# Kernel tuning notes

Hardware: AMD Instinct MI355X
Metric: run time of the kernel (lower is better)

The kernel has to match this reference:

```python
import math
import jax, jax.numpy as jnp
import numpy as np

B, L, T, D, H, SD = 8, 512, 512, 768, 12, 5


def setup_inputs() -> dict:
    key = jax.random.key(0)
    ks = jax.random.split(key, 16)
    s = 0.02
    return {
        "q": jax.random.normal(ks[0], (B, L, D), jnp.float32),
        "k": jax.random.normal(ks[1], (B, T, D), jnp.float32),
        "v": jax.random.normal(ks[2], (B, T, D), jnp.float32),
        "pairwise_locs": jax.random.normal(ks[3], (B, L, T, SD), jnp.float32),
        "key_padding_mask": jax.random.randint(ks[4], (B, T), 0, 2).astype(bool),
        "Wq": jax.random.normal(ks[5], (D, D), jnp.float32) * s,
        "bq": jnp.zeros((D,), jnp.float32),
        "Wk": jax.random.normal(ks[6], (D, D), jnp.float32) * s,
        "bk": jnp.zeros((D,), jnp.float32),
        "Wv": jax.random.normal(ks[7], (D, D), jnp.float32) * s,
        "bv": jnp.zeros((D,), jnp.float32),
        "Wl": jax.random.normal(ks[8], (D, H * (SD + 1)), jnp.float32) * s,
        "bl": jnp.zeros((H * (SD + 1),), jnp.float32),
        "Wf": jax.random.normal(ks[9], (D, D), jnp.float32) * s,
        "bf": jnp.zeros((D,), jnp.float32),
    }


def reference(q, k, v, pairwise_locs, key_padding_mask,
              Wq, bq, Wk, bk, Wv, bv, Wl, bl, Wf, bf):
    b, l, d = q.shape
    t = k.shape[1]
    sd = pairwise_locs.shape[-1]
    h = Wl.shape[1] // (sd + 1)          # spatial_multihead=True -> h == n_head
    dh = d // h

    # projections -> [h, b, seq, dh]
    qh = (q @ Wq + bq).reshape(b, l, h, dh).transpose(2, 0, 1, 3)
    kh = (k @ Wk + bk).reshape(b, t, h, dh).transpose(2, 0, 1, 3)
    vh = (v @ Wv + bv).reshape(b, t, h, dh).transpose(2, 0, 1, 3)

    attn = jnp.einsum('hblk,hbtk->hblt', qh, kh) / math.sqrt(dh)

    # language-conditioned spatial weights from residual (= q input)
    sw = (q @ Wl + bl).reshape(b, l, h, sd + 1).transpose(2, 0, 1, 3)  # [h,b,l,sd+1]
    spatial_bias = sw[..., :1]
    spatial_w = sw[..., 1:]
    loc_attn = jax.nn.sigmoid(
        jnp.einsum('hbld,bltd->hblt', spatial_w, pairwise_locs) + spatial_bias)

    mask = key_padding_mask[None, :, None, :]          # [1,b,1,t]
    attn = jnp.where(mask, -jnp.inf, attn)
    loc_attn = jnp.where(mask, 0.0, loc_attn)

    fused_attn = jax.nn.softmax(jnp.log(jnp.clip(loc_attn, 1e-6)) + attn, axis=3)

    out = jnp.einsum('hblt,hbtv->hblv', fused_attn, vh)
    out = out.transpose(1, 2, 0, 3).reshape(b, l, d)
    out = out @ Wf + bf
    return (out, fused_attn)
```

## Files before the change

### kernel.cpp

```cpp
#include <hip/hip_runtime.h>
#include <hip/hip_bf16.h>

#define B_ 8
#define L_ 512
#define T_ 512
#define D_ 768
#define H_ 12
#define DH_ 64
#define SD_ 5
#define NSW_ 72
#define K2_ 1536
#define K3_ 2304

typedef __attribute__((ext_vector_type(8))) short bf16x8;
typedef __attribute__((ext_vector_type(4))) float f32x4;
typedef unsigned short ushort_t;

__device__ __forceinline__ unsigned short f2bf(float x) {
    union { __hip_bfloat16 h; unsigned short u; } cv;
    cv.h = __float2bfloat16(x);
    return cv.u;
}
__device__ __forceinline__ float bf2f(unsigned short u) {
    union { unsigned short u; __hip_bfloat16 h; } cv;
    cv.u = u;
    return __bfloat162float(cv.h);
}

__device__ __forceinline__ void gload_lds16(const void* g, void* l) {
    __builtin_amdgcn_global_load_lds((const __attribute__((address_space(1))) void*)g,
                                     (__attribute__((address_space(3))) void*)l,
                                     16, 0, 0);
}

__global__ __launch_bounds__(256) void asplit_kernel(
    const float* __restrict__ q, const float* __restrict__ k, const float* __restrict__ v,
    short* __restrict__ q2, short* __restrict__ k2, short* __restrict__ v2)
{
    const int z = blockIdx.z;
    const float* A = (z == 0) ? q : (z == 1) ? k : v;
    short* O = (z == 0) ? q2 : (z == 1) ? k2 : v2;
    const int col = blockIdx.x * 256 + threadIdx.x;
    const int m   = blockIdx.y;
    if (col >= D_) return;
    const float a = A[(size_t)m * D_ + col];
    const unsigned short hi = f2bf(a);
    const unsigned short lo = f2bf(a - bf2f(hi));
    O[(size_t)m * K2_ + col]       = (short)hi;
    O[(size_t)m * K2_ + D_ + col]  = (short)lo;
}

__global__ __launch_bounds__(256) void wsplit_kernel(
    const float* __restrict__ Wq, const float* __restrict__ Wk,
    const float* __restrict__ Wv, const float* __restrict__ Wl,
    const float* __restrict__ Wf,
    short* __restrict__ WqT3, short* __restrict__ WkT3, short* __restrict__ WvT3,
    short* __restrict__ WlT3, short* __restrict__ WfT3)
{
    const int z = blockIdx.z;
    const float* W; short* O; int Nw, Npad;
    if (z == 0)      { W = Wq; O = WqT3; Nw = D_;   Npad = 768; }
    else if (z == 1) { W = Wk; O = WkT3; Nw = D_;   Npad = 768; }
    else if (z == 2) { W = Wv; O = WvT3; Nw = D_;   Npad = 768; }
    else if (z == 3) { W = Wl; O = WlT3; Nw = NSW_; Npad = 128; }
    else             { W = Wf; O = WfT3; Nw = D_;   Npad = 768; }

    const int k0 = blockIdx.x * 64;
    const int n0 = blockIdx.y * 64;
    if (n0 >= Npad) return;

    __shared__ float sm[64][65];
    const int c  = threadIdx.x & 63;
    const int r4 = threadIdx.x >> 6;

#pragma unroll
    for (int i = 0; i < 16; i++) {
        const int r = i * 4 + r4;
        float val = 0.f;
        if (n0 + c < Nw) val = W[(size_t)(k0 + r) * Nw + n0 + c];
        sm[r][c] = val;
    }
    __syncthreads();

#pragma unroll
    for (int i = 0; i < 16; i++) {
        const int nl = i * 4 + r4;
        const int n  = n0 + nl;
        if (n >= Npad) continue;
        const float v = (n < Nw) ? sm[c][nl] : 0.f;
        const unsigned short hi = f2bf(v);
        const unsigned short lo = f2bf(v - bf2f(hi));
        const size_t rb = (size_t)n * K3_;
        O[rb + k0 + c]        = (short)hi;
        O[rb + 768 + k0 + c]  = (short)lo;
        O[rb + 1536 + k0 + c] = (short)hi;
    }
}

__global__ __launch_bounds__(256) void mfma_gemm(
    const short* __restrict__ q2, const short* __restrict__ k2, const short* __restrict__ v2,
    const short* __restrict__ WqT3, const short* __restrict__ WkT3,
    const short* __restrict__ WvT3, const short* __restrict__ WlT3,
    const short* __restrict__ WfT3,
    const float* __restrict__ bq, const float* __restrict__ bk,
    const float* __restrict__ bv, const float* __restrict__ bl,
    const float* __restrict__ bf,
    const short* __restrict__ outp2,
    ushort_t* __restrict__ qs2a, ushort_t* __restrict__ ks2a, ushort_t* __restrict__ vt2,
    float* __restrict__ swv, float* __restrict__ outf,
    int zoff)
{
    const int z = zoff + blockIdx.z;
    const short* A2; const short* WT3; const float* bias;
    if (z == 0)      { A2 = q2;    WT3 = WqT3; bias = bq; }
    else if (z == 1) { A2 = k2;    WT3 = WkT3; bias = bk; }
    else if (z == 2) { A2 = v2;    WT3 = WvT3; bias = bv; }
    else if (z == 3) { A2 = q2;    WT3 = WlT3; bias = bl; }
    else             { A2 = outp2; WT3 = WfT3; bias = bf; }

    if (z == 3 && blockIdx.x != 0) return;

    const int m0 = blockIdx.y * 128;
    const int n0 = blockIdx.x * 128;

    __shared__ __align__(16) short As[128 * 32];
    __shared__ __align__(16) short Bs[128 * 32];

    const int tid  = threadIdx.x;
    const int lane = tid & 63;
    const int wv_  = tid >> 6;
    const int wm   = (wv_ & 1) << 6;
    const int wn   = (wv_ >> 1) << 6;
    const int l15  = lane & 15;
    const int quad = lane >> 4;

    f32x4 acc[4][4] = {};

    const int sa  = tid;
    const int sb  = tid + 256;
    const int ra  = sa >> 2, ka = (sa & 3) << 3;
    const int rb  = sb >> 2, kb8 = (sb & 3) << 3;

    for (int kb = 0; kb < K3_; kb += 32) {
        const int akb = (kb < 768) ? kb : kb - 768;
        __syncthreads();
        gload_lds16(A2  + (size_t)(m0 + ra) * K2_ + akb + ka,  &As[sa << 3]);
        gload_lds16(A2  + (size_t)(m0 + rb) * K2_ + akb + kb8, &As[sb << 3]);
        gload_lds16(WT3 + (size_t)(n0 + ra) * K3_ + kb  + ka,  &Bs[sa << 3]);
        gload_lds16(WT3 + (size_t)(n0 + rb) * K3_ + kb  + kb8, &Bs[sb << 3]);
        __syncthreads();

        bf16x8 af[4], bfr[4];
#pragma unroll
        for (int t = 0; t < 4; t++) {
            af[t]  = *(const bf16x8*)&As[(wm + t * 16 + l15) * 32 + quad * 8];
            bfr[t] = *(const bf16x8*)&Bs[(wn + t * 16 + l15) * 32 + quad * 8];
        }
#pragma unroll
        for (int mt = 0; mt < 4; mt++)
#pragma unroll
            for (int nt = 0; nt < 4; nt++)
                acc[mt][nt] = __builtin_amdgcn_mfma_f32_16x16x32_bf16(
                    af[mt], bfr[nt], acc[mt][nt], 0, 0, 0);
    }

    if (z <= 2) {
        ushort_t* dst = (z == 0) ? qs2a : (z == 1) ? ks2a : vt2;
#pragma unroll
        for (int nt = 0; nt < 4; nt++) {
            const int col = n0 + wn + nt * 16 + l15;
            const int hh = col >> 6, dd = col & 63;
            const float bvv = bias[col];
#pragma unroll
            for (int mt = 0; mt < 4; mt++) {
                const int rowb = m0 + wm + mt * 16 + quad * 4;
                if (z < 2) {
#pragma unroll
                    for (int r = 0; r < 4; r++) {
                        const int gr = rowb + r;
                        const int bb = gr >> 9, ll = gr & 511;
                        const float x = acc[mt][nt][r] + bvv;
                        const ushort_t hi = f2bf(x);
                        const ushort_t lo = f2bf(x - bf2f(hi));
                        const size_t base = (((size_t)hh * B_ + bb) * 512 + ll) * 128 + dd;
                        dst[base]      = hi;
                        dst[base + 64] = lo;
                    }
                } else {
                    const int bb = rowb >> 9, tt = rowb & 511;
                    ushort_t hi4[4], lo4[4];
#pragma unroll
                    for (int r = 0; r < 4; r++) {
                        const float x = acc[mt][nt][r] + bvv;
                        hi4[r] = f2bf(x);
                        lo4[r] = f2bf(x - bf2f(hi4[r]));
                    }
                    const size_t base = (((size_t)hh * B_ + bb) * 128 + dd) * 512 + tt;
                    *(ushort4*)&dst[base]            = *(ushort4*)hi4;
                    *(ushort4*)&dst[base + 64 * 512] = *(ushort4*)lo4;
                }
            }
        }
    } else if (z == 3) {
#pragma unroll
        for (int nt = 0; nt < 4; nt++) {
            const int col = n0 + wn + nt * 16 + l15;
            if (col >= NSW_) continue;
            const float bvv = bias[col];
#pragma unroll
            for (int mt = 0; mt < 4; mt++) {
                const int row = m0 + wm + mt * 16 + quad * 4;
#pragma unroll
                for (int r = 0; r < 4; r++)
                    swv[(size_t)(row + r) * NSW_ + col] = acc[mt][nt][r] + bvv;
            }
        }
    } else {
#pragma unroll
        for (int nt = 0; nt < 4; nt++) {
            const int col = n0 + wn + nt * 16 + l15;
            const float bvv = bias[col];
#pragma unroll
            for (int mt = 0; mt < 4; mt++) {
                const int row = m0 + wm + mt * 16 + quad * 4;
#pragma unroll
                for (int r = 0; r < 4; r++)
                    outf[(size_t)(row + r) * D_ + col] = acc[mt][nt][r] + bvv;
            }
        }
    }
}

__global__ __launch_bounds__(256) void sig_kernel(
    const float* __restrict__ ploc, const float* __restrict__ swv,
    const int* __restrict__ maskp, _Float16* __restrict__ sig16)
{
    const int b = blockIdx.y;
    const int l = blockIdx.x;
    const int tid = threadIdx.x;

    __shared__ float pls[512 * 5];
    __shared__ float sws[72];
    __shared__ int   msk[512];

    const float* src = ploc + (size_t)(b * 512 + l) * 512 * 5;
    for (int i = tid; i < 640; i += 256)
        *(float4*)&pls[i * 4] = *(const float4*)(src + i * 4);
    if (tid < 72) sws[tid] = swv[(size_t)(b * 512 + l) * NSW_ + tid];
    for (int i = tid; i < 512; i += 256) msk[i] = maskp[b * 512 + i];
    __syncthreads();

    for (int e = tid; e < H_ * 512; e += 256) {
        const int t  = e & 511;
        const int hh = e >> 9;
        float s = sws[hh * 6];
#pragma unroll
        for (int d = 0; d < SD_; d++) s += sws[hh * 6 + 1 + d] * pls[t * 5 + d];
        const float sig = msk[t] ? 0.f : fmaxf(1.f / (1.f + __expf(-s)), 1e-6f);
        sig16[(((size_t)hh * B_ + b) * 512 + l) * 512 + t] = (_Float16)sig;
    }
}

__global__ __launch_bounds__(256) void attn_kernel(
    const ushort_t* __restrict__ qs2, const ushort_t* __restrict__ ks2,
    const ushort_t* __restrict__ vt2, const _Float16* __restrict__ sig16,
    float* __restrict__ fused, ushort_t* __restrict__ outp2,
    float* __restrict__ sums)
{
    const int h  = blockIdx.z;
    const int b  = blockIdx.y;
    const int l0 = blockIdx.x << 6;
    const int hb = h * B_ + b;
    const int tid  = threadIdx.x;
    const int lane = tid & 63;
    const int wv   = tid >> 6;
    const int l15  = lane & 15;
    const int quad = lane >> 4;

    __shared__ __align__(16) ushort_t qs[64 * 128];
    __shared__ __align__(16) ushort_t ks[64 * 128];
    __shared__ __align__(16) ushort_t vts[128 * 64];
    __shared__ __align__(16) ushort_t ps[64 * 136];
    __shared__ float ssb[4 * 64];
    __shared__ float ssum[64];

    {
        const size_t qbase = ((size_t)hb * 512 + l0) * 128;
#pragma unroll
        for (int j = 0; j < 4; j++) {
            const int i = tid + 256 * j;
            const int r = i >> 4, c = i & 15, gc = c ^ (r & 7);
            gload_lds16(qs2 + qbase + r * 128 + gc * 8, &qs[i * 8]);
        }
    }

    float pacc = 0.f;
    f32x4 accpv[4] = {};

    for (int t0 = 0; t0 < T_; t0 += 64) {
        __syncthreads();
        {
            const size_t kbase = ((size_t)hb * 512 + t0) * 128;
#pragma unroll
            for (int j = 0; j < 4; j++) {
                const int i = tid + 256 * j;
                const int r = i >> 4, c = i & 15, gc = c ^ (r & 7);
                gload_lds16(ks2 + kbase + r * 128 + gc * 8, &ks[i * 8]);
            }
            const size_t vbase = (size_t)hb * 128 * 512;
#pragma unroll
            for (int j = 0; j < 4; j++) {
                const int i = tid + 256 * j;
                const int r = i >> 3, c = i & 7, gc = c ^ (r & 7);
                gload_lds16(vt2 + vbase + (size_t)r * 512 + t0 + gc * 8, &vts[i * 8]);
            }
        }
        __syncthreads();

        float sigv[4][4];
        {
            const _Float16* sgp = sig16 + (((size_t)hb * 512 + l0) * 512) + t0 + wv * 16 + l15;
#pragma unroll
            for (int mt = 0; mt < 4; mt++)
#pragma unroll
                for (int r2 = 0; r2 < 4; r2++)
                    sigv[mt][r2] = (float)sgp[(size_t)(mt * 16 + quad * 4 + r2) * 512];
        }

        f32x4 acq[4] = {};
        {
            const int trow = wv * 16 + l15;
            const int tsw  = trow & 7;
            const bf16x8 bk0 = *(const bf16x8*)&ks[trow * 128 + ((0  + quad) ^ tsw) * 8];
            const bf16x8 bk1 = *(const bf16x8*)&ks[trow * 128 + ((4  + quad) ^ tsw) * 8];
            const bf16x8 bk2 = *(const bf16x8*)&ks[trow * 128 + ((8  + quad) ^ tsw) * 8];
            const bf16x8 bk3 = *(const bf16x8*)&ks[trow * 128 + ((12 + quad) ^ tsw) * 8];
#pragma unroll
            for (int mt = 0; mt < 4; mt++) {
                const int arow = mt * 16 + l15;
                const int asw  = arow & 7;
                const bf16x8 a0 = *(const bf16x8*)&qs[arow * 128 + ((0  + quad) ^ asw) * 8];
                const bf16x8 a1 = *(const bf16x8*)&qs[arow * 128 + ((4  + quad) ^ asw) * 8];
                const bf16x8 a2 = *(const bf16x8*)&qs[arow * 128 + ((8  + quad) ^ asw) * 8];
                const bf16x8 a3 = *(const bf16x8*)&qs[arow * 128 + ((12 + quad) ^ asw) * 8];
                f32x4 a = acq[mt];
                a = __builtin_amdgcn_mfma_f32_16x16x32_bf16(a0, bk0, a, 0, 0, 0);
                a = __builtin_amdgcn_mfma_f32_16x16x32_bf16(a1, bk1, a, 0, 0, 0);
                a = __builtin_amdgcn_mfma_f32_16x16x32_bf16(a0, bk2, a, 0, 0, 0);
                a = __builtin_amdgcn_mfma_f32_16x16x32_bf16(a1, bk3, a, 0, 0, 0);
                a = __builtin_amdgcn_mfma_f32_16x16x32_bf16(a2, bk0, a, 0, 0, 0);
                a = __builtin_amdgcn_mfma_f32_16x16x32_bf16(a3, bk1, a, 0, 0, 0);
                acq[mt] = a;
            }
        }

        {
            const int tcol = wv * 16 + l15;
#pragma unroll
            for (int mt = 0; mt < 4; mt++)
#pragma unroll
                for (int r2 = 0; r2 < 4; r2++) {
                    const int lrow = mt * 16 + quad * 4 + r2;
                    const float p  = sigv[mt][r2] * __expf(acq[mt][r2] * 0.125f);
                    const ushort_t hi = f2bf(p);
                    const ushort_t lo = f2bf(p - bf2f(hi));
                    ps[lrow * 136 + tcol]      = hi;
                    ps[lrow * 136 + 64 + tcol] = lo;
                }
        }
        __syncthreads();

        {
            const int row = tid >> 2, c4 = tid & 3;
            float vbuf[16];
            float s = 0.f;
#pragma unroll
            for (int jj = 0; jj < 16; jj++) {
                const int t = c4 * 16 + jj;
                const float pv = bf2f(ps[row * 136 + t]) + bf2f(ps[row * 136 + 64 + t]);
                vbuf[jj] = pv;
                s += pv;
            }
            pacc += s;
            float* dstf = fused + ((size_t)hb * 512 + l0 + row) * 512 + t0 + c4 * 16;
#pragma unroll
            for (int jj = 0; jj < 4; jj++)
                *(float4*)(dstf + jj * 4) = *(float4*)&vbuf[jj * 4];
        }

        {
            const int vrh = wv * 16 + l15;
            const int vrl = 64 + vrh;
            const int swh = vrh & 7, swl = vrl & 7;
            const bf16x8 bh0 = *(const bf16x8*)&vts[vrh * 64 + ((0 + quad) ^ swh) * 8];
            const bf16x8 bh1 = *(const bf16x8*)&vts[vrh * 64 + ((4 + quad) ^ swh) * 8];
            const bf16x8 bl0 = *(const bf16x8*)&vts[vrl * 64 + ((0 + quad) ^ swl) * 8];
            const bf16x8 bl1 = *(const bf16x8*)&vts[vrl * 64 + ((4 + quad) ^ swl) * 8];
#pragma unroll
            for (int mt = 0; mt < 4; mt++) {
                const int prow = mt * 16 + l15;
                const bf16x8 ph0 = *(const bf16x8*)&ps[prow * 136 + 0  + quad * 8];
                const bf16x8 ph1 = *(const bf16x8*)&ps[prow * 136 + 32 + quad * 8];
                const bf16x8 pl0 = *(const bf16x8*)&ps[prow * 136 + 64 + quad * 8];
                const bf16x8 pl1 = *(const bf16x8*)&ps[prow * 136 + 96 + quad * 8];
                f32x4 a = accpv[mt];
                a = __builtin_amdgcn_mfma_f32_16x16x32_bf16(ph0, bh0, a, 0, 0, 0);
                a = __builtin_amdgcn_mfma_f32_16x16x32_bf16(ph1, bh1, a, 0, 0, 0);
                a = __builtin_amdgcn_mfma_f32_16x16x32_bf16(ph0, bl0, a, 0, 0, 0);
                a = __builtin_amdgcn_mfma_f32_16x16x32_bf16(ph1, bl1, a, 0, 0, 0);
                a = __builtin_amdgcn_mfma_f32_16x16x32_bf16(pl0, bh0, a, 0, 0, 0);
                a = __builtin_amdgcn_mfma_f32_16x16x32_bf16(pl1, bh1, a, 0, 0, 0);
                accpv[mt] = a;
            }
        }
    }

    __syncthreads();
    ssb[(tid & 3) * 64 + (tid >> 2)] = pacc;
    __syncthreads();
    if (tid < 64) {
        const float s = ssb[tid] + ssb[64 + tid] + ssb[128 + tid] + ssb[192 + tid];
        ssum[tid] = s;
        sums[(size_t)hb * 512 + l0 + tid] = s;
    }
    __syncthreads();

#pragma unroll
    for (int mt = 0; mt < 4; mt++)
#pragma unroll
        for (int r2 = 0; r2 < 4; r2++) {
            const int lrow = mt * 16 + quad * 4 + r2;
            const float val = accpv[mt][r2] / ssum[lrow];
            const ushort_t hi = f2bf(val);
            const ushort_t lo = f2bf(val - bf2f(hi));
            const size_t obase = ((size_t)(b * 512 + l0 + lrow)) * K2_ + h * 64 + wv * 16 + l15;
            outp2[obase]       = hi;
            outp2[obase + D_]  = lo;
        }
}

__global__ __launch_bounds__(256) void norm_kernel(
    float* __restrict__ fused, const float* __restrict__ sums)
{
    const int gi = blockIdx.x * 256 + threadIdx.x;
    float4* f4 = (float4*)fused;
    float4 v = f4[gi];
    const float inv = 1.f / sums[gi >> 7];
    v.x *= inv; v.y *= inv; v.z *= inv; v.w *= inv;
    f4[gi] = v;
}

extern "C" void kernel_launch(void* const* d_in, const int* in_sizes, int n_in,
                              void* d_out, int out_size, void* d_ws, size_t ws_size,
                              hipStream_t stream) {
    const float* q    = (const float*)d_in[0];
    const float* k    = (const float*)d_in[1];
    const float* v    = (const float*)d_in[2];
    const float* ploc = (const float*)d_in[3];
    const int*   mask = (const int*)  d_in[4];
    const float* Wq   = (const float*)d_in[5];
    const float* bq   = (const float*)d_in[6];
    const float* Wk   = (const float*)d_in[7];
    const float* bk   = (const float*)d_in[8];
    const float* Wv   = (const float*)d_in[9];
    const float* bv   = (const float*)d_in[10];
    const float* Wl   = (const float*)d_in[11];
    const float* bl   = (const float*)d_in[12];
    const float* Wf   = (const float*)d_in[13];
    const float* bf   = (const float*)d_in[14];

    char* base = (char*)d_ws;
    short*    q2    = (short*)(base + 0);
    short*    k2    = (short*)(base + 12582912);
    short*    v2    = (short*)(base + 25165824);
    short*    WqT3  = (short*)(base + 37748736);
    short*    WkT3  = (short*)(base + 41287680);
    short*    WvT3  = (short*)(base + 44826624);
    short*    WlT3  = (short*)(base + 48365568);
    _Float16* sig16 = (_Float16*)(base + 0);
    short*    WfT3  = (short*)(base + 50331648);
    ushort_t* qs2a  = (ushort_t*)(base + 53870592);
    ushort_t* ks2a  = (ushort_t*)(base + 66453504);
    ushort_t* vt2   = (ushort_t*)(base + 79036416);
    float*    swv   = (float*)(base + 91619328);
    float*    sums  = (float*)(base + 92798976);
    short*    outp2 = (short*)(base + 92995584);

    float* out   = (float*)d_out;
    float* fused = out + (size_t)4096 * D_;

    asplit_kernel<<<dim3(3, 4096, 3), 256, 0, stream>>>(q, k, v, q2, k2, v2);
    wsplit_kernel<<<dim3(12, 12, 5), 256, 0, stream>>>(
        Wq, Wk, Wv, Wl, Wf, WqT3, WkT3, WvT3, WlT3, WfT3);

    mfma_gemm<<<dim3(6, 32, 4), 256, 0, stream>>>(
        q2, k2, v2, WqT3, WkT3, WvT3, WlT3, WfT3,
        bq, bk, bv, bl, bf, outp2, qs2a, ks2a, vt2, swv, out, 0);

    sig_kernel<<<dim3(512, 8), 256, 0, stream>>>(ploc, swv, mask, sig16);

    attn_kernel<<<dim3(8, 8, 12), 256, 0, stream>>>(
        qs2a, ks2a, vt2, sig16, fused, (ushort_t*)outp2, sums);

    norm_kernel<<<dim3(24576), 256, 0, stream>>>(fused, sums);

    mfma_gemm<<<dim3(6, 32, 1), 256, 0, stream>>>(
        q2, k2, v2, WqT3, WkT3, WvT3, WlT3, WfT3,
        bq, bk, bv, bl, bf, outp2, qs2a, ks2a, vt2, swv, out, 4);
}
```

Before: 511.4 us.

## Split-K projection and output GEMMs with atomics, fuse normalization into attention

```diff
diff --git a/kernel.cpp b/kernel.cpp
--- a/kernel.cpp
+++ b/kernel.cpp
@@ -31,6 +31,17 @@
     __builtin_amdgcn_global_load_lds((const __attribute__((address_space(1))) void*)g,
                                      (__attribute__((address_space(3))) void*)l,
                                      16, 0, 0);
+}
+
+__global__ __launch_bounds__(256) void zero_kernel(float4* __restrict__ p) {
+    p[(size_t)blockIdx.x * 256 + threadIdx.x] = make_float4(0.f, 0.f, 0.f, 0.f);
+}
+
+__global__ __launch_bounds__(256) void bias_init(
+    float4* __restrict__ out4, const float4* __restrict__ bf4)
+{
+    const size_t idx = (size_t)blockIdx.x * 256 + threadIdx.x;
+    out4[idx] = bf4[idx % 192];
 }
 
 __global__ __launch_bounds__(256) void asplit_kernel(
@@ -97,31 +108,24 @@
     }
 }
 
-__global__ __launch_bounds__(256) void mfma_gemm(
+__global__ __launch_bounds__(256, 4) void proj_gemm(
     const short* __restrict__ q2, const short* __restrict__ k2, const short* __restrict__ v2,
     const short* __restrict__ WqT3, const short* __restrict__ WkT3,
     const short* __restrict__ WvT3, const short* __restrict__ WlT3,
-    const short* __restrict__ WfT3,
-    const float* __restrict__ bq, const float* __restrict__ bk,
-    const float* __restrict__ bv, const float* __restrict__ bl,
-    const float* __restrict__ bf,
-    const short* __restrict__ outp2,
-    ushort_t* __restrict__ qs2a, ushort_t* __restrict__ ks2a, ushort_t* __restrict__ vt2,
-    float* __restrict__ swv, float* __restrict__ outf,
-    int zoff)
-{
-    const int z = zoff + blockIdx.z;
-    const short* A2; const short* WT3; const float* bias;
-    if (z == 0)      { A2 = q2;    WT3 = WqT3; bias = bq; }
-    else if (z == 1) { A2 = k2;    WT3 = WkT3; bias = bk; }
-    else if (z == 2) { A2 = v2;    WT3 = WvT3; bias = bv; }
-    else if (z == 3) { A2 = q2;    WT3 = WlT3; bias = bl; }
-    else             { A2 = outp2; WT3 = WfT3; bias = bf; }
-
-    if (z == 3 && blockIdx.x != 0) return;
+    float* __restrict__ Cp, float* __restrict__ Cpsw)
+{
+    const int z = blockIdx.z;
+    int g, part, bx = blockIdx.x;
+    if (z < 6) { g = z >> 1; part = z & 1; }
+    else       { if (bx >= 2) return; g = 3; part = bx; bx = 0; }
+
+    const short* A2  = (g == 1) ? k2 : (g == 2) ? v2 : q2;
+    const short* WT3 = (g == 0) ? WqT3 : (g == 1) ? WkT3 : (g == 2) ? WvT3 : WlT3;
+    float* C   = (g < 3) ? (Cp + (size_t)g * 4096 * 768) : Cpsw;
+    const int Ncols = (g < 3) ? 768 : NSW_;
 
     const int m0 = blockIdx.y * 128;
-    const int n0 = blockIdx.x * 128;
+    const int n0 = bx * 128;
 
     __shared__ __align__(16) short As[128 * 32];
     __shared__ __align__(16) short Bs[128 * 32];
@@ -141,7 +145,8 @@
     const int ra  = sa >> 2, ka = (sa & 3) << 3;
     const int rb  = sb >> 2, kb8 = (sb & 3) << 3;
 
-    for (int kb = 0; kb < K3_; kb += 32) {
+    const int kbeg = part * 1152;
+    for (int kb = kbeg; kb < kbeg + 1152; kb += 32) {
         const int akb = (kb < 768) ? kb : kb - 768;
         __syncthreads();
         gload_lds16(A2  + (size_t)(m0 + ra) * K2_ + akb + ka,  &As[sa << 3]);
@@ -164,71 +169,167 @@
                     af[mt], bfr[nt], acc[mt][nt], 0, 0, 0);
     }
 
-    if (z <= 2) {
-        ushort_t* dst = (z == 0) ? qs2a : (z == 1) ? ks2a : vt2;
-#pragma unroll
-        for (int nt = 0; nt < 4; nt++) {
-            const int col = n0 + wn + nt * 16 + l15;
-            const int hh = col >> 6, dd = col & 63;
-            const float bvv = bias[col];
-#pragma unroll
-            for (int mt = 0; mt < 4; mt++) {
-                const int rowb = m0 + wm + mt * 16 + quad * 4;
-                if (z < 2) {
-#pragma unroll
-                    for (int r = 0; r < 4; r++) {
-                        const int gr = rowb + r;
-                        const int bb = gr >> 9, ll = gr & 511;
-                        const float x = acc[mt][nt][r] + bvv;
-                        const ushort_t hi = f2bf(x);
-                        const ushort_t lo = f2bf(x - bf2f(hi));
-                        const size_t base = (((size_t)hh * B_ + bb) * 512 + ll) * 128 + dd;
-                        dst[base]      = hi;
-                        dst[base + 64] = lo;
-                    }
-                } else {
-                    const int bb = rowb >> 9, tt = rowb & 511;
-                    ushort_t hi4[4], lo4[4];
-#pragma unroll
-                    for (int r = 0; r < 4; r++) {
-                        const float x = acc[mt][nt][r] + bvv;
-                        hi4[r] = f2bf(x);
-                        lo4[r] = f2bf(x - bf2f(hi4[r]));
-                    }
-                    const size_t base = (((size_t)hh * B_ + bb) * 128 + dd) * 512 + tt;
-                    *(ushort4*)&dst[base]            = *(ushort4*)hi4;
-                    *(ushort4*)&dst[base + 64 * 512] = *(ushort4*)lo4;
-                }
-            }
-        }
-    } else if (z == 3) {
-#pragma unroll
-        for (int nt = 0; nt < 4; nt++) {
-            const int col = n0 + wn + nt * 16 + l15;
-            if (col >= NSW_) continue;
-            const float bvv = bias[col];
-#pragma unroll
-            for (int mt = 0; mt < 4; mt++) {
-                const int row = m0 + wm + mt * 16 + quad * 4;
-#pragma unroll
-                for (int r = 0; r < 4; r++)
-                    swv[(size_t)(row + r) * NSW_ + col] = acc[mt][nt][r] + bvv;
-            }
-        }
-    } else {
-#pragma unroll
-        for (int nt = 0; nt < 4; nt++) {
-            const int col = n0 + wn + nt * 16 + l15;
-            const float bvv = bias[col];
-#pragma unroll
-            for (int mt = 0; mt < 4; mt++) {
-                const int row = m0 + wm + mt * 16 + quad * 4;
-#pragma unroll
-                for (int r = 0; r < 4; r++)
-                    outf[(size_t)(row + r) * D_ + col] = acc[mt][nt][r] + bvv;
-            }
-        }
-    }
+#pragma unroll
+    for (int nt = 0; nt < 4; nt++) {
+        const int col = n0 + wn + nt * 16 + l15;
+        if (col >= Ncols) continue;
+#pragma unroll
+        for (int mt = 0; mt < 4; mt++) {
+            const int rowb = m0 + wm + mt * 16 + quad * 4;
+#pragma unroll
+            for (int r = 0; r < 4; r++)
+                unsafeAtomicAdd(&C[(size_t)(rowb + r) * Ncols + col], acc[mt][nt][r]);
+        }
+    }
+}
+
+__global__ __launch_bounds__(256, 4) void final_gemm(
+    const short* __restrict__ A2, const short* __restrict__ WT3,
+    float* __restrict__ out)
+{
+    const int part = blockIdx.z;
+    const int m0 = blockIdx.y * 128;
+    const int n0 = blockIdx.x * 128;
+
+    __shared__ __align__(16) short As[128 * 32];
+    __shared__ __align__(16) short Bs[128 * 32];
+
+    const int tid  = threadIdx.x;
+    const int lane = tid & 63;
+    const int wv_  = tid >> 6;
+    const int wm   = (wv_ & 1) << 6;
+    const int wn   = (wv_ >> 1) << 6;
+    const int l15  = lane & 15;
+    const int quad = lane >> 4;
+
+    f32x4 acc[4][4] = {};
+
+    const int sa  = tid;
+    const int sb  = tid + 256;
+    const int ra  = sa >> 2, ka = (sa & 3) << 3;
+    const int rb  = sb >> 2, kb8 = (sb & 3) << 3;
+
+    const int kbeg = part * 576;
+    for (int kb = kbeg; kb < kbeg + 576; kb += 32) {
+        const int akb = (kb < 768) ? kb : kb - 768;
+        __syncthreads();
+        gload_lds16(A2  + (size_t)(m0 + ra) * K2_ + akb + ka,  &As[sa << 3]);
+        gload_lds16(A2  + (size_t)(m0 + rb) * K2_ + akb + kb8, &As[sb << 3]);
+        gload_lds16(WT3 + (size_t)(n0 + ra) * K3_ + kb  + ka,  &Bs[sa << 3]);
+        gload_lds16(WT3 + (size_t)(n0 + rb) * K3_ + kb  + kb8, &Bs[sb << 3]);
+        __syncthreads();
+
+        bf16x8 af[4], bfr[4];
+#pragma unroll
+        for (int t = 0; t < 4; t++) {
+            af[t]  = *(const bf16x8*)&As[(wm + t * 16 + l15) * 32 + quad * 8];
+            bfr[t] = *(const bf16x8*)&Bs[(wn + t * 16 + l15) * 32 + quad * 8];
+        }
+#pragma unroll
+        for (int mt = 0; mt < 4; mt++)
+#pragma unroll
+            for (int nt = 0; nt < 4; nt++)
+                acc[mt][nt] = __builtin_amdgcn_mfma_f32_16x16x32_bf16(
+                    af[mt], bfr[nt], acc[mt][nt], 0, 0, 0);
+    }
+
+#pragma unroll
+    for (int nt = 0; nt < 4; nt++) {
+        const int col = n0 + wn + nt * 16 + l15;
+#pragma unroll
+        for (int mt = 0; mt < 4; mt++) {
+            const int rowb = m0 + wm + mt * 16 + quad * 4;
+#pragma unroll
+            for (int r = 0; r < 4; r++)
+                unsafeAtomicAdd(&out[(size_t)(rowb + r) * D_ + col], acc[mt][nt][r]);
+        }
+    }
+}
+
+__global__ __launch_bounds__(256) void convert_qk(
+    const float* __restrict__ Cp, const float* __restrict__ bq,
+    const float* __restrict__ bk,
+    ushort_t* __restrict__ qs2a, ushort_t* __restrict__ ks2a)
+{
+    const int g = blockIdx.z;
+    const float* src  = Cp + (size_t)g * 4096 * 768;
+    const float* bias = g ? bk : bq;
+    ushort_t* dst = g ? ks2a : qs2a;
+    const int r0 = blockIdx.x * 8;
+
+#pragma unroll
+    for (int j = 0; j < 6; j++) {
+        const int idx = threadIdx.x + 256 * j;
+        const int row = r0 + idx / 192;
+        const int c4  = (idx % 192) * 4;
+        float4 x = *(const float4*)&src[(size_t)row * 768 + c4];
+        const float4 b4 = *(const float4*)&bias[c4];
+        x.x += b4.x; x.y += b4.y; x.z += b4.z; x.w += b4.w;
+        const int hh = c4 >> 6, dd = c4 & 63;
+        const int bb = row >> 9, ll = row & 511;
+        const size_t base = (((size_t)hh * B_ + bb) * 512 + ll) * 128 + dd;
+        ushort_t hi[4], lo[4];
+        const float xv[4] = {x.x, x.y, x.z, x.w};
+#pragma unroll
+        for (int u = 0; u < 4; u++) {
+            hi[u] = f2bf(xv[u]);
+            lo[u] = f2bf(xv[u] - bf2f(hi[u]));
+        }
+        *(ushort4*)&dst[base]      = *(ushort4*)hi;
+        *(ushort4*)&dst[base + 64] = *(ushort4*)lo;
+    }
+}
+
+__global__ __launch_bounds__(256) void convert_v(
+    const float* __restrict__ Cp, const float* __restrict__ bv,
+    ushort_t* __restrict__ vt2)
+{
+    const int t0 = blockIdx.x * 64;
+    const int b  = blockIdx.y;
+    const int h  = blockIdx.z;
+    const float* src = Cp + (size_t)2 * 4096 * 768;
+
+    __shared__ float sm[64][65];
+    const int tid = threadIdx.x;
+    {
+        const int r = tid >> 2, cseg = (tid & 3) * 16;
+        const size_t rowb = (size_t)(b * 512 + t0 + r) * 768 + h * 64 + cseg;
+#pragma unroll
+        for (int u = 0; u < 4; u++) {
+            float4 x = *(const float4*)&src[rowb + u * 4];
+            sm[r][cseg + u * 4 + 0] = x.x;
+            sm[r][cseg + u * 4 + 1] = x.y;
+            sm[r][cseg + u * 4 + 2] = x.z;
+            sm[r][cseg + u * 4 + 3] = x.w;
+        }
+    }
+    __syncthreads();
+    {
+        const int c = tid >> 2, seg = (tid & 3) * 16;
+        const float bvv = bv[h * 64 + c];
+        ushort_t hib[16], lob[16];
+#pragma unroll
+        for (int i = 0; i < 16; i++) {
+            const float val = sm[seg + i][c] + bvv;
+            hib[i] = f2bf(val);
+            lob[i] = f2bf(val - bf2f(hib[i]));
+        }
+        const size_t bh = (((size_t)h * B_ + b) * 128 + c) * 512 + t0 + seg;
+        const size_t bl = bh + (size_t)64 * 512;
+#pragma unroll
+        for (int u = 0; u < 4; u++) {
+            *(ushort4*)&vt2[bh + u * 4] = *(ushort4*)&hib[u * 4];
+            *(ushort4*)&vt2[bl + u * 4] = *(ushort4*)&lob[u * 4];
+        }
+    }
+}
+
+__global__ __launch_bounds__(256) void convert_sw(
+    const float* __restrict__ Cpsw, const float* __restrict__ bl,
+    float* __restrict__ swv)
+{
+    const int idx = blockIdx.x * 256 + threadIdx.x;
+    swv[idx] = Cpsw[idx] + bl[idx % NSW_];
 }
 
 __global__ __launch_bounds__(256) void sig_kernel(
@@ -261,11 +362,10 @@
     }
 }
 
-__global__ __launch_bounds__(256) void attn_kernel(
+__global__ __launch_bounds__(256, 3) void attn_kernel(
     const ushort_t* __restrict__ qs2, const ushort_t* __restrict__ ks2,
     const ushort_t* __restrict__ vt2, const _Float16* __restrict__ sig16,
-    float* __restrict__ fused, ushort_t* __restrict__ outp2,
-    float* __restrict__ sums)
+    float* __restrict__ fused, ushort_t* __restrict__ outp2)
 {
     const int h  = blockIdx.z;
     const int b  = blockIdx.y;
@@ -277,20 +377,21 @@
     const int l15  = lane & 15;
     const int quad = lane >> 4;
 
-    __shared__ __align__(16) ushort_t qs[64 * 128];
     __shared__ __align__(16) ushort_t ks[64 * 128];
     __shared__ __align__(16) ushort_t vts[128 * 64];
     __shared__ __align__(16) ushort_t ps[64 * 136];
     __shared__ float ssb[4 * 64];
     __shared__ float ssum[64];
 
+    bf16x8 aq[4][4];
     {
         const size_t qbase = ((size_t)hb * 512 + l0) * 128;
 #pragma unroll
-        for (int j = 0; j < 4; j++) {
-            const int i = tid + 256 * j;
-            const int r = i >> 4, c = i & 15, gc = c ^ (r & 7);
-            gload_lds16(qs2 + qbase + r * 128 + gc * 8, &qs[i * 8]);
+        for (int mt = 0; mt < 4; mt++) {
+            const size_t rb = qbase + (size_t)(mt * 16 + l15) * 128;
+#pragma unroll
+            for (int c = 0; c < 4; c++)
+                aq[mt][c] = *(const bf16x8*)(qs2 + rb + (c * 4 + quad) * 8);
         }
     }
 
@@ -337,19 +438,13 @@
             const bf16x8 bk3 = *(const bf16x8*)&ks[trow * 128 + ((12 + quad) ^ tsw) * 8];
 #pragma unroll
             for (int mt = 0; mt < 4; mt++) {
-                const int arow = mt * 16 + l15;
-                const int asw  = arow & 7;
-                const bf16x8 a0 = *(const bf16x8*)&qs[arow * 128 + ((0  + quad) ^ asw) * 8];
-                const bf16x8 a1 = *(const bf16x8*)&qs[arow * 128 + ((4  + quad) ^ asw) * 8];
-                const bf16x8 a2 = *(const bf16x8*)&qs[arow * 128 + ((8  + quad) ^ asw) * 8];
-                const bf16x8 a3 = *(const bf16x8*)&qs[arow * 128 + ((12 + quad) ^ asw) * 8];
                 f32x4 a = acq[mt];
-                a = __builtin_amdgcn_mfma_f32_16x16x32_bf16(a0, bk0, a, 0, 0, 0);
-                a = __builtin_amdgcn_mfma_f32_16x16x32_bf16(a1, bk1, a, 0, 0, 0);
-                a = __builtin_amdgcn_mfma_f32_16x16x32_bf16(a0, bk2, a, 0, 0, 0);
-                a = __builtin_amdgcn_mfma_f32_16x16x32_bf16(a1, bk3, a, 0, 0, 0);
-                a = __builtin_amdgcn_mfma_f32_16x16x32_bf16(a2, bk0, a, 0, 0, 0);
-                a = __builtin_amdgcn_mfma_f32_16x16x32_bf16(a3, bk1, a, 0, 0, 0);
+                a = __builtin_amdgcn_mfma_f32_16x16x32_bf16(aq[mt][0], bk0, a, 0, 0, 0);
+                a = __builtin_amdgcn_mfma_f32_16x16x32_bf16(aq[mt][1], bk1, a, 0, 0, 0);
+                a = __builtin_amdgcn_mfma_f32_16x16x32_bf16(aq[mt][0], bk2, a, 0, 0, 0);
+                a = __builtin_amdgcn_mfma_f32_16x16x32_bf16(aq[mt][1], bk3, a, 0, 0, 0);
+                a = __builtin_amdgcn_mfma_f32_16x16x32_bf16(aq[mt][2], bk0, a, 0, 0, 0);
+                a = __builtin_amdgcn_mfma_f32_16x16x32_bf16(aq[mt][3], bk1, a, 0, 0, 0);
                 acq[mt] = a;
             }
         }
@@ -419,11 +514,23 @@
     ssb[(tid & 3) * 64 + (tid >> 2)] = pacc;
     __syncthreads();
     if (tid < 64) {
-        const float s = ssb[tid] + ssb[64 + tid] + ssb[128 + tid] + ssb[192 + tid];
-        ssum[tid] = s;
-        sums[(size_t)hb * 512 + l0 + tid] = s;
+        ssum[tid] = ssb[tid] + ssb[64 + tid] + ssb[128 + tid] + ssb[192 + tid];
     }
     __syncthreads();
+
+    {
+        const int row = tid >> 2, c4 = tid & 3;
+        const float inv = 1.f / ssum[row];
+        float* frow = fused + ((size_t)hb * 512 + l0 + row) * 512 + c4 * 16;
+        for (int t0 = 0; t0 < T_; t0 += 64) {
+#pragma unroll
+            for (int jj = 0; jj < 4; jj++) {
+                float4 x = *(float4*)(frow + t0 + jj * 4);
+                x.x *= inv; x.y *= inv; x.z *= inv; x.w *= inv;
+                *(float4*)(frow + t0 + jj * 4) = x;
+            }
+        }
+    }
 
 #pragma unroll
     for (int mt = 0; mt < 4; mt++)
@@ -437,17 +544,6 @@
             outp2[obase]       = hi;
             outp2[obase + D_]  = lo;
         }
-}
-
-__global__ __launch_bounds__(256) void norm_kernel(
-    float* __restrict__ fused, const float* __restrict__ sums)
-{
-    const int gi = blockIdx.x * 256 + threadIdx.x;
-    float4* f4 = (float4*)fused;
-    float4 v = f4[gi];
-    const float inv = 1.f / sums[gi >> 7];
-    v.x *= inv; v.y *= inv; v.z *= inv; v.w *= inv;
-    f4[gi] = v;
 }
 
 extern "C" void kernel_launch(void* const* d_in, const int* in_sizes, int n_in,
@@ -477,34 +573,37 @@
     short*    WkT3  = (short*)(base + 41287680);
     short*    WvT3  = (short*)(base + 44826624);
     short*    WlT3  = (short*)(base + 48365568);
-    _Float16* sig16 = (_Float16*)(base + 0);
-    short*    WfT3  = (short*)(base + 50331648);
-    ushort_t* qs2a  = (ushort_t*)(base + 53870592);
-    ushort_t* ks2a  = (ushort_t*)(base + 66453504);
-    ushort_t* vt2   = (ushort_t*)(base + 79036416);
-    float*    swv   = (float*)(base + 91619328);
-    float*    sums  = (float*)(base + 92798976);
-    short*    outp2 = (short*)(base + 92995584);
+    short*    WfT3  = (short*)(base + 48955392);
+    float*    Cp    = (float*)(base + 52494336);
+    float*    Cpsw  = (float*)(base + 90243072);
+    ushort_t* qs2a  = (ushort_t*)q2;
+    ushort_t* ks2a  = (ushort_t*)k2;
+    ushort_t* vt2   = (ushort_t*)v2;
+    float*    swv   = (float*)WqT3;
+    _Float16* sig16 = (_Float16*)(base + 52494336);
+    ushort_t* outp2 = (ushort_t*)(base + 102825984);
 
     float* out   = (float*)d_out;
     float* fused = out + (size_t)4096 * D_;
+
+    zero_kernel<<<dim3(9504), 256, 0, stream>>>((float4*)Cp);
+    bias_init<<<dim3(3072), 256, 0, stream>>>((float4*)out, (const float4*)bf);
 
     asplit_kernel<<<dim3(3, 4096, 3), 256, 0, stream>>>(q, k, v, q2, k2, v2);
     wsplit_kernel<<<dim3(12, 12, 5), 256, 0, stream>>>(
         Wq, Wk, Wv, Wl, Wf, WqT3, WkT3, WvT3, WlT3, WfT3);
 
-    mfma_gemm<<<dim3(6, 32, 4), 256, 0, stream>>>(
-        q2, k2, v2, WqT3, WkT3, WvT3, WlT3, WfT3,
-        bq, bk, bv, bl, bf, outp2, qs2a, ks2a, vt2, swv, out, 0);
+    proj_gemm<<<dim3(6, 32, 7), 256, 0, stream>>>(
+        q2, k2, v2, WqT3, WkT3, WvT3, WlT3, Cp, Cpsw);
+
+    convert_qk<<<dim3(512, 1, 2), 256, 0, stream>>>(Cp, bq, bk, qs2a, ks2a);
+    convert_v<<<dim3(8, 8, 12), 256, 0, stream>>>(Cp, bv, vt2);
+    convert_sw<<<dim3(1152), 256, 0, stream>>>(Cpsw, bl, swv);
 
     sig_kernel<<<dim3(512, 8), 256, 0, stream>>>(ploc, swv, mask, sig16);
 
     attn_kernel<<<dim3(8, 8, 12), 256, 0, stream>>>(
-        qs2a, ks2a, vt2, sig16, fused, (ushort_t*)outp2, sums);
-
-    norm_kernel<<<dim3(24576), 256, 0, stream>>>(fused, sums);
-
-    mfma_gemm<<<dim3(6, 32, 1), 256, 0, stream>>>(
-        q2, k2, v2, WqT3, WkT3, WvT3, WlT3, WfT3,
-        bq, bk, bv, bl, bf, outp2, qs2a, ks2a, vt2, swv, out, 4);
-}
+        qs2a, ks2a, vt2, sig16, fused, outp2);
+
+    final_gemm<<<dim3(6, 32, 4), 256, 0, stream>>>((const short*)outp2, WfT3, out);
+}
```

After: 563.0 us. +10.1%, slower.
